# Optimization experiments

Measured on AMD Instinct MI355X. Metric: run time of the kernel, lower is better.

## Reference

```python
import jax, jax.numpy as jnp
import numpy as np

B, T, K = 512, 1024, 48


def setup_inputs() -> dict:
    key = jax.random.key(0)
    k1, k2, k3, k4, k5, k6 = jax.random.split(key, 6)
    return {
        "emission_scores": jax.random.normal(k1, (B, T, K), dtype=jnp.float32),
        "lengths": jax.random.randint(k2, (B,), 1, T + 1, dtype=jnp.int64),
        "tags": jax.random.randint(k3, (B, T), 0, K, dtype=jnp.int64),
        "prior": 0.1 * jax.random.normal(k4, (K,), dtype=jnp.float32),
        "transition": 0.1 * jax.random.normal(k5, (K, K), dtype=jnp.float32),
        "final_transition": 0.1 * jax.random.normal(k6, (K,), dtype=jnp.float32),
    }


def _partition_function(emission_scores, lengths, prior, transition, final_transition):
    batch, timesteps, num_tags = emission_scores.shape
    # alpha_0[b, i] = emis[b, 0, i] + prior[i]
    alpha0 = emission_scores[:, 0, :] + prior[None, :]

    def step(prev_alpha, emis_t):
        # alpha_t[b, i] = logsumexp_j(prev_alpha[b, j] + transition[i, j]) + emis_t[b, i]
        a = jax.nn.logsumexp(prev_alpha[:, None, :] + transition[None, :, :], axis=2)
        a = a + emis_t
        return a, a

    emis_rest = jnp.swapaxes(emission_scores, 0, 1)[1:]  # [T-1, B, K]
    _, alphas = jax.lax.scan(step, alpha0, emis_rest)
    alphas = jnp.concatenate([alpha0[None], alphas], axis=0)  # [T, B, K]
    alpha_final = alphas[lengths - 1, jnp.arange(batch)]  # [B, K] at last valid step
    alpha_final = alpha_final + final_transition[None, :]
    return jax.nn.logsumexp(alpha_final, axis=1)


def _score_path(emission_scores, lengths, tags, prior, transition, final_transition):
    batch, timesteps, num_tags = emission_scores.shape
    emis_tag = jnp.take_along_axis(emission_scores, tags[:, :, None], axis=2)[..., 0]  # [B, T]
    trans = transition[tags[:, 1:], tags[:, :-1]]  # [B, T-1]
    pr = prior[tags[:, 0]][:, None]  # [B, 1]
    scores = jnp.concatenate([pr, trans], axis=1) + emis_tag  # [B, T]
    valid = jnp.arange(timesteps)[None, :] < lengths[:, None]  # True for t < length
    scores = jnp.where(valid, scores, 0.0)
    final_tags = tags[jnp.arange(batch), lengths - 1]
    return jnp.sum(scores, axis=1) + final_transition[final_tags]


def reference(emission_scores, lengths, tags, prior, transition, final_transition):
    lengths = jnp.clip(lengths, 1, None)
    logZ = _partition_function(emission_scores, lengths, prior, transition, final_transition)
    path = _score_path(emission_scores, lengths, tags, prior, transition, final_transition)
    return jnp.mean(logZ - path)
```

## Files before the change

### kernel.cpp

```cpp
#include <hip/hip_runtime.h>


#define BB    512
#define TT    1024
#define KK    48
#define GG    16
#define NGRP  32
#define NSLOT 16
#define SLOTB (KK * GG * 4)
#define PHASE 8
#define NPROD 3
#define BLKT  256

typedef __attribute__((ext_vector_type(4))) short bf16x4;
typedef __attribute__((ext_vector_type(4))) float f32x4;

__device__ __forceinline__ f32x4 mfma16(bf16x4 a, bf16x4 b, f32x4 c) {
#if __has_builtin(__builtin_amdgcn_mfma_f32_16x16x16bf16_1k)
    return __builtin_amdgcn_mfma_f32_16x16x16bf16_1k(a, b, c, 0, 0, 0);
#else
    f32x4 d;
    asm volatile("v_mfma_f32_16x16x16_bf16 %0, %1, %2, %3"
                 : "=v"(d) : "v"(a), "v"(b), "v"(c));
    return d;
#endif
}

#if __has_builtin(__builtin_amdgcn_cvt_pk_bf16_f32)
typedef __attribute__((ext_vector_type(2))) __bf16 bf16x2_v;
__device__ __forceinline__ unsigned pk2(float lo, float hi) {
    union { bf16x2_v v; unsigned u; } x;
    x.v = __builtin_amdgcn_cvt_pk_bf16_f32(lo, hi);
    return x.u;
}
#else
__device__ __forceinline__ unsigned pk2(float lo, float hi) {
    return __builtin_amdgcn_perm(__float_as_uint(hi) + 0x8000u,
                                 __float_as_uint(lo) + 0x8000u,
                                 0x07060302u);
}
#endif
__device__ __forceinline__ bf16x4 pack4(float a, float b, float c, float d) {
    union { unsigned u[2]; bf16x4 v; } x;
    x.u[0] = pk2(a, b);
    x.u[1] = pk2(c, d);
    return x.v;
}

__device__ __forceinline__ float wave_reduce_sum(float v) {
    #pragma unroll
    for (int off = 32; off > 0; off >>= 1)
        v += __shfl_xor(v, off, 64);
    return v;
}

__global__ __launch_bounds__(BLKT, 1) void crf_main_kernel(
    const float* __restrict__ emis,
    const int*   __restrict__ lengths,
    const int*   __restrict__ tags,
    const float* __restrict__ prior,
    const float* __restrict__ trans,
    const float* __restrict__ finalT,
    float*       __restrict__ ws)
{
    __shared__ __align__(16) unsigned char ring[NSLOT * SLOTB];
    __shared__ int prodCnt[NPROD];
    __shared__ int consCnt;

    const int tid  = threadIdx.x;
    const int wv   = tid >> 6;
    const int lane = tid & 63;

    if (blockIdx.x >= NGRP) {
        const int b = blockIdx.x - NGRP;
        int len = lengths[b];
        len = (len < 1) ? 1 : (len > TT ? TT : len);
        const float* eb = emis + (size_t)b * TT * KK;
        const int*   tg = tags + (size_t)b * TT;
        float ps = 0.0f;
        for (int t = tid; t < len; t += BLKT) {
            int cur = tg[t];
            float ev = eb[(size_t)t * KK + cur];
            float tr = (t == 0) ? prior[cur] : trans[cur * KK + tg[t - 1]];
            ps += ev + tr;
        }
        ps = wave_reduce_sum(ps);
        float* red = (float*)ring;
        if (lane == 0) red[wv] = ps;
        __syncthreads();
        if (tid == 0)
            ws[BB + b] = red[0] + red[1] + red[2] + red[3] + finalT[tg[len - 1]];
        return;
    }

    const int g = blockIdx.x;

    if (tid == 0) {
        prodCnt[0] = 0; prodCnt[1] = 0; prodCnt[2] = 0; consCnt = 0;
    }
    __syncthreads();

    int myLen = lengths[g * GG + (lane & 15)];
    myLen = (myLen < 1) ? 1 : (myLen > TT ? TT : myLen);
    int gmax = myLen;
    #pragma unroll
    for (int off = 32; off > 0; off >>= 1) {
        int o = __shfl_xor(gmax, off, 64);
        gmax = (o > gmax) ? o : gmax;
    }
    const int nsteps = gmax - 1;
    const int nphase = (nsteps + PHASE - 1) / PHASE;

    if (wv >= 1) {
        size_t go[3]; int lo16[3];
        #pragma unroll
        for (int j = 0; j < 3; ++j) {
            int idx = lane + 64 * j;
            int s   = idx / 12;
            int kg  = idx - s * 12;
            go[j]   = (size_t)(g * GG + s) * (TT * KK) + kg * 4;
            lo16[j] = idx * 16;
        }
        const int sA = wv - 1;
        float4 L[9];

#define PLOAD(KP)                                                          \
        {                                                                  \
            _Pragma("unroll")                                              \
            for (int h = 0; h < 3; ++h) {                                  \
                int s = sA + 3 * h;                                        \
                if (s < PHASE) {                                           \
                    int t  = 1 + (KP) * PHASE + s;                         \
                    int tc = (t > nsteps) ? nsteps : t;                    \
                    _Pragma("unroll")                                      \
                    for (int j = 0; j < 3; ++j)                            \
                        L[h*3+j] = *reinterpret_cast<const float4*>(       \
                            emis + go[j] + (size_t)tc * KK);               \
                }                                                          \
            }                                                              \
        }

        PLOAD(0);
        volatile int* vc = &consCnt;
        for (int k = 0; k < nphase; ++k) {
            while (*vc < k - 1) __builtin_amdgcn_s_sleep(1);
            asm volatile("" ::: "memory");
            #pragma unroll
            for (int h = 0; h < 3; ++h) {
                int s = sA + 3 * h;
                if (s < PHASE) {
                    int t = 1 + k * PHASE + s;
                    unsigned char* bp = &ring[(t & (NSLOT - 1)) * SLOTB];
                    #pragma unroll
                    for (int j = 0; j < 3; ++j) {
                        float4 l = L[h*3+j];
                        float4 e;
                        e.x = __expf(l.x); e.y = __expf(l.y);
                        e.z = __expf(l.z); e.w = __expf(l.w);
                        *reinterpret_cast<float4*>(bp + lo16[j]) = e;
                    }
                }
            }
            __threadfence_block();
            if (lane == 0) *(volatile int*)&prodCnt[sA] = k + 1;
            PLOAD(k + 1);
        }
#undef PLOAD
        return;
    }

    const int col   = lane & 15;
    const int grp   = lane >> 4;
    const int rbase = grp * 4;
    const int seq   = g * GG + col;
    const int lenn1 = myLen - 1;

    bf16x4 A[3][3];
    #pragma unroll
    for (int mt = 0; mt < 3; ++mt) {
        #pragma unroll
        for (int kt = 0; kt < 3; ++kt) {
            float4 tv = *reinterpret_cast<const float4*>(
                trans + (size_t)(mt * 16 + col) * KK + kt * 16 + rbase);
            A[mt][kt] = pack4(__expf(tv.x), __expf(tv.y),
                              __expf(tv.z), __expf(tv.w));
        }
    }

    float expF[12];
    #pragma unroll
    for (int mt = 0; mt < 3; ++mt) {
        float4 fv = *reinterpret_cast<const float4*>(finalT + mt * 16 + rbase);
        expF[mt*4+0] = __expf(fv.x); expF[mt*4+1] = __expf(fv.y);
        expF[mt*4+2] = __expf(fv.z); expF[mt*4+3] = __expf(fv.w);
    }

    const float* ebase = emis + (size_t)seq * TT * KK + rbase;

    float w[12];
    float c;
    float zcap = 0.0f;
    {
        float a0[12];
        #pragma unroll
        for (int mt = 0; mt < 3; ++mt) {
            float4 ev = *reinterpret_cast<const float4*>(ebase + mt * 16);
            float4 pv = *reinterpret_cast<const float4*>(prior + mt * 16 + rbase);
            a0[mt*4+0] = ev.x + pv.x;
            a0[mt*4+1] = ev.y + pv.y;
            a0[mt*4+2] = ev.z + pv.z;
            a0[mt*4+3] = ev.w + pv.w;
        }
        float mx = a0[0];
        #pragma unroll
        for (int r = 1; r < 12; ++r) mx = fmaxf(mx, a0[r]);
        mx = fmaxf(mx, __shfl_xor(mx, 16, 64));
        mx = fmaxf(mx, __shfl_xor(mx, 32, 64));
        c = mx;
        #pragma unroll
        for (int r = 0; r < 12; ++r) w[r] = __expf(a0[r] - c);
        if (__ballot(lenn1 == 0)) {
            float S = 0.0f;
            #pragma unroll
            for (int r = 0; r < 12; ++r) S = fmaf(w[r], expF[r], S);
            S += __shfl_xor(S, 16, 64);
            S += __shfl_xor(S, 32, 64);
            if (lenn1 == 0) zcap = c + __logf(S);
        }
    }

    bf16x4 Bt[3];
    Bt[0] = pack4(w[0], w[1], w[2],  w[3]);
    Bt[1] = pack4(w[4], w[5], w[6],  w[7]);
    Bt[2] = pack4(w[8], w[9], w[10], w[11]);

    const int foff = col * 48 + grp * 4;
    const f32x4 zero4 = {0.f, 0.f, 0.f, 0.f};
    volatile int* vp = prodCnt;

    for (int k = 0; k < nphase; ++k) {
        while (vp[0] < k + 1 || vp[1] < k + 1 || vp[2] < k + 1)
            __builtin_amdgcn_s_sleep(1);
        asm volatile("" ::: "memory");
        #pragma unroll
        for (int s8 = 0; s8 < PHASE; ++s8) {
            const int t = 1 + k * PHASE + s8;
            const float* sp = reinterpret_cast<const float*>(
                &ring[(t & (NSLOT - 1)) * SLOTB]) + foff;
            float4 X0 = *reinterpret_cast<const float4*>(sp);
            float4 X1 = *reinterpret_cast<const float4*>(sp + 16);
            float4 X2 = *reinterpret_cast<const float4*>(sp + 32);

            f32x4 D0 = mfma16(A[0][0], Bt[0], zero4);
            f32x4 D1 = mfma16(A[1][0], Bt[0], zero4);
            f32x4 D2 = mfma16(A[2][0], Bt[0], zero4);
            D0 = mfma16(A[0][1], Bt[1], D0);
            D1 = mfma16(A[1][1], Bt[1], D1);
            D2 = mfma16(A[2][1], Bt[1], D2);
            D0 = mfma16(A[0][2], Bt[2], D0);
            D1 = mfma16(A[1][2], Bt[2], D1);
            D2 = mfma16(A[2][2], Bt[2], D2);

            w[0]  = D0.x * X0.x;  w[1]  = D0.y * X0.y;
            w[2]  = D0.z * X0.z;  w[3]  = D0.w * X0.w;
            w[4]  = D1.x * X1.x;  w[5]  = D1.y * X1.y;
            w[6]  = D1.z * X1.z;  w[7]  = D1.w * X1.w;
            w[8]  = D2.x * X2.x;  w[9]  = D2.y * X2.y;
            w[10] = D2.z * X2.z;  w[11] = D2.w * X2.w;

            if ((t & 7) == 0) {
                float mx = w[0];
                #pragma unroll
                for (int r = 1; r < 12; ++r) mx = fmaxf(mx, w[r]);
                mx = fmaxf(mx, __shfl_xor(mx, 16, 64));
                mx = fmaxf(mx, __shfl_xor(mx, 32, 64));
                c += __logf(mx);
                float rm = __builtin_amdgcn_rcpf(mx);
                #pragma unroll
                for (int r = 0; r < 12; ++r) w[r] *= rm;
            }

            if (__ballot(t == lenn1)) {
                float S = 0.0f;
                #pragma unroll
                for (int r = 0; r < 12; ++r) S = fmaf(w[r], expF[r], S);
                S += __shfl_xor(S, 16, 64);
                S += __shfl_xor(S, 32, 64);
                if (t == lenn1) zcap = c + __logf(S);
            }

            Bt[0] = pack4(w[0], w[1], w[2],  w[3]);
            Bt[1] = pack4(w[4], w[5], w[6],  w[7]);
            Bt[2] = pack4(w[8], w[9], w[10], w[11]);
        }
        __threadfence_block();
        asm volatile("" ::: "memory");
        if (lane == 0) *(volatile int*)&consCnt = k + 1;
    }

    if (lane < GG) ws[seq] = zcap;
}

__global__ __launch_bounds__(512) void reduce_mean_kernel(
    const float* __restrict__ ws, float* __restrict__ out)
{
    __shared__ float sm[8];
    int tid = threadIdx.x;
    float x = ws[tid] - ws[BB + tid];
    x = wave_reduce_sum(x);
    if ((tid & 63) == 0) sm[tid >> 6] = x;
    __syncthreads();
    if (tid < 8) {
        float y = sm[tid];
        y += __shfl_xor(y, 1, 64);
        y += __shfl_xor(y, 2, 64);
        y += __shfl_xor(y, 4, 64);
        if (tid == 0) out[0] = y * (1.0f / 512.0f);
    }
}

extern "C" void kernel_launch(void* const* d_in, const int* in_sizes, int n_in,
                              void* d_out, int out_size, void* d_ws, size_t ws_size,
                              hipStream_t stream) {
    const float* emis    = (const float*)d_in[0];
    const int*   lengths = (const int*)  d_in[1];
    const int*   tags    = (const int*)  d_in[2];
    const float* prior   = (const float*)d_in[3];
    const float* trans   = (const float*)d_in[4];
    const float* finalT  = (const float*)d_in[5];

    float* ws  = (float*)d_ws;
    float* out = (float*)d_out;

    crf_main_kernel<<<NGRP + BB, BLKT, 0, stream>>>(emis, lengths, tags, prior,
                                                    trans, finalT, ws);
    reduce_mean_kernel<<<1, 512, 0, stream>>>(ws, out);
}
```

Baseline: 331.6 us.

## Pad LDS ring rows to 52 floats and prefetch next step's emissions

Each per-sequence row of the LDS emission ring is padded from 48 to 52 floats (13 float4 slots), so producer writes and consumer reads no longer collide on the same LDS banks. The consumer loop also loads the next timestep's emission values from LDS one iteration ahead, which hides LDS latency behind the MFMA chain. The cost is a slightly larger ring footprint and extra live registers for the prefetched values.

```diff
diff --git a/kernel.cpp b/kernel.cpp
--- a/kernel.cpp
+++ b/kernel.cpp
@@ -7,7 +7,7 @@
 #define GG    16
 #define NGRP  32
 #define NSLOT 16
-#define SLOTB (KK * GG * 4)
+#define SLOTB (13 * GG * 16)
 #define PHASE 8
 #define NPROD 3
 #define BLKT  256
@@ -115,11 +115,11 @@
         size_t go[3]; int lo16[3];
         #pragma unroll
         for (int j = 0; j < 3; ++j) {
-            int idx = lane + 64 * j;
-            int s   = idx / 12;
-            int kg  = idx - s * 12;
-            go[j]   = (size_t)(g * GG + s) * (TT * KK) + kg * 4;
-            lo16[j] = idx * 16;
+            int lidx = lane + 64 * j;
+            int s    = lidx / 12;
+            int kg   = lidx - s * 12;
+            go[j]    = (size_t)(g * GG + s) * (TT * KK) + kg * 4;
+            lo16[j]  = (s * 13 + kg) * 16;
         }
         const int sA = wv - 1;
         float4 L[9];
@@ -234,7 +234,7 @@
     Bt[1] = pack4(w[4], w[5], w[6],  w[7]);
     Bt[2] = pack4(w[8], w[9], w[10], w[11]);
 
-    const int foff = col * 48 + grp * 4;
+    const int foff = col * 52 + grp * 4;
     const f32x4 zero4 = {0.f, 0.f, 0.f, 0.f};
     volatile int* vp = prodCnt;
 
@@ -242,14 +242,23 @@
         while (vp[0] < k + 1 || vp[1] < k + 1 || vp[2] < k + 1)
             __builtin_amdgcn_s_sleep(1);
         asm volatile("" ::: "memory");
+        const int t0 = 1 + k * PHASE;
+        const float* sp0 = reinterpret_cast<const float*>(
+            &ring[(t0 & (NSLOT - 1)) * SLOTB]) + foff;
+        float4 Xa = *reinterpret_cast<const float4*>(sp0);
+        float4 Xb = *reinterpret_cast<const float4*>(sp0 + 16);
+        float4 Xc = *reinterpret_cast<const float4*>(sp0 + 32);
         #pragma unroll
         for (int s8 = 0; s8 < PHASE; ++s8) {
-            const int t = 1 + k * PHASE + s8;
-            const float* sp = reinterpret_cast<const float*>(
-                &ring[(t & (NSLOT - 1)) * SLOTB]) + foff;
-            float4 X0 = *reinterpret_cast<const float4*>(sp);
-            float4 X1 = *reinterpret_cast<const float4*>(sp + 16);
-            float4 X2 = *reinterpret_cast<const float4*>(sp + 32);
+            const int t = t0 + s8;
+            float4 X0 = Xa, X1 = Xb, X2 = Xc;
+            if (s8 + 1 < PHASE) {
+                const float* spn = reinterpret_cast<const float*>(
+                    &ring[((t + 1) & (NSLOT - 1)) * SLOTB]) + foff;
+                Xa = *reinterpret_cast<const float4*>(spn);
+                Xb = *reinterpret_cast<const float4*>(spn + 16);
+                Xc = *reinterpret_cast<const float4*>(spn + 32);
+            }
 
             f32x4 D0 = mfma16(A[0][0], Bt[0], zero4);
             f32x4 D1 = mfma16(A[1][0], Bt[0], zero4);
```

New measurement: 330.1 us. About the same (-0.5%).
